# Kernel optimization log

Measured on AMD Instinct MI355X. Metric: run time of the kernel, lower is better.

## Reference

```python
import jax, jax.numpy as jnp
import numpy as np
import math

D_MODEL = 1024
N_HEADS = 16
HEAD_DIM = 64


def setup_inputs() -> dict:
    key = jax.random.key(0)
    k_x, k_q, k_k, k_v, k_o = jax.random.split(key, 5)
    lecun = jax.nn.initializers.lecun_normal()
    return {
        "x": jax.random.normal(k_x, (4, 2048, D_MODEL), dtype=jnp.float32),
        "W_q": lecun(k_q, (N_HEADS, D_MODEL, HEAD_DIM), jnp.float32),
        "W_k": lecun(k_k, (N_HEADS, D_MODEL, HEAD_DIM), jnp.float32),
        "W_v": lecun(k_v, (N_HEADS, D_MODEL, HEAD_DIM), jnp.float32),
        "W_o": lecun(k_o, (D_MODEL, D_MODEL), jnp.float32),
    }


def reference(x, W_q, W_k, W_v, W_o):
    # x: [b, l, e]; W_{q,k,v}: [h, e, d]; W_o: [e, e]
    q = jnp.einsum('ble,hed->bhld', x, W_q)
    k = jnp.einsum('ble,hed->bhld', x, W_k)
    v = jnp.einsum('ble,hed->bhld', x, W_v)
    scores = jnp.einsum('bhld,bhsd->bhls', q, k) / math.sqrt(HEAD_DIM)
    attn = jax.nn.softmax(scores, axis=-1)
    av = jnp.einsum('bhls,bhsd->bhld', attn, v)  # [b, h, l, d]
    b, h, l, d = av.shape
    concat = jnp.transpose(av, (0, 2, 1, 3)).reshape(b, l, h * d)
    out = jnp.einsum('ble,eo->blo', concat, W_o)
    return jnp.asarray(out, dtype=jnp.float32)
```

## Files before the change

### kernel.cpp

```cpp
#include <hip/hip_runtime.h>

#define BATCH 4
#define LSEQ  2048
#define DM    1024
#define NH    16
#define HD    64
#define NTOK  (BATCH * LSEQ)

typedef _Float16 f16x8 __attribute__((ext_vector_type(8)));
typedef _Float16 f16x4 __attribute__((ext_vector_type(4)));
typedef __fp16   hf16x2 __attribute__((ext_vector_type(2)));
typedef float    f32x4 __attribute__((ext_vector_type(4)));
typedef float    f32x16 __attribute__((ext_vector_type(16)));

typedef __attribute__((address_space(1))) const unsigned int GU32;
typedef __attribute__((address_space(3))) unsigned int LU32;

__device__ __forceinline__ void gload_lds16(const _Float16* g, _Float16* l)
{
    __builtin_amdgcn_global_load_lds(
        (GU32*)(unsigned long long)g,
        (LU32*)(unsigned int)(unsigned long long)l, 16, 0, 0);
}


__global__ __launch_bounds__(256) void cvt_kernel(const float* __restrict__ src,
                                                  _Float16* __restrict__ dst, int n4)
{
    int i = blockIdx.x * 256 + threadIdx.x;
    if (i >= n4) return;
    float4 v = ((const float4*)src)[i];
    f16x4 h;
    h[0] = (_Float16)v.x; h[1] = (_Float16)v.y; h[2] = (_Float16)v.z; h[3] = (_Float16)v.w;
    ((f16x4*)dst)[i] = h;
}

__global__ __launch_bounds__(256) void tconv3_kernel(
    const float* __restrict__ Wq, const float* __restrict__ Wk,
    const float* __restrict__ Wv, _Float16* __restrict__ dst)
{
    const int z = blockIdx.z;
    const int which = z >> 4, h = z & 15;
    const float* __restrict__ src =
        ((which == 0) ? Wq : (which == 1) ? Wk : Wv) + (size_t)h * DM * HD;
    _Float16* __restrict__ d = dst + (size_t)z * DM * HD;
    const int e0 = blockIdx.y * 64;
    __shared__ float Ls[64][65];
    const int t = threadIdx.x;
    #pragma unroll
    for (int j = 0; j < 4; ++j) {
        int cidx = t + j * 256;
        int row = cidx >> 4, col4 = (cidx & 15) * 4;
        float4 v = *(const float4*)&src[(size_t)(e0 + row) * HD + col4];
        Ls[row][col4] = v.x; Ls[row][col4+1] = v.y; Ls[row][col4+2] = v.z; Ls[row][col4+3] = v.w;
    }
    __syncthreads();
    const int dd = t & 63, sc = t >> 6;
    alignas(16) _Float16 tmp[16];
    #pragma unroll
    for (int i = 0; i < 16; ++i) tmp[i] = (_Float16)Ls[sc * 16 + i][dd];
    *(f16x8*)&d[(size_t)dd * DM + e0 + sc * 16]     = *(f16x8*)&tmp[0];
    *(f16x8*)&d[(size_t)dd * DM + e0 + sc * 16 + 8] = *(f16x8*)&tmp[8];
}

__global__ __launch_bounds__(256) void tconv_kernel(const float* __restrict__ src,
                                                    _Float16* __restrict__ dst, int E, int D)
{
    const int d0 = blockIdx.x * 64, e0 = blockIdx.y * 64;
    __shared__ float Ls[64][65];
    const int t = threadIdx.x;
    #pragma unroll
    for (int j = 0; j < 4; ++j) {
        int cidx = t + j * 256;
        int row = cidx >> 4, col4 = (cidx & 15) * 4;
        float4 v = *(const float4*)&src[(size_t)(e0 + row) * D + d0 + col4];
        Ls[row][col4] = v.x; Ls[row][col4+1] = v.y; Ls[row][col4+2] = v.z; Ls[row][col4+3] = v.w;
    }
    __syncthreads();
    const int dd = t & 63, sc = t >> 6;
    alignas(16) _Float16 tmp[16];
    #pragma unroll
    for (int i = 0; i < 16; ++i) tmp[i] = (_Float16)Ls[sc * 16 + i][dd];
    *(f16x8*)&dst[(size_t)(d0 + dd) * E + e0 + sc * 16]     = *(f16x8*)&tmp[0];
    *(f16x8*)&dst[(size_t)(d0 + dd) * E + e0 + sc * 16 + 8] = *(f16x8*)&tmp[8];
}

template<int MODE>
__global__ __launch_bounds__(256) void gemm_kernel(
    const _Float16* __restrict__ A, const _Float16* __restrict__ B,
    float* __restrict__ out32,
    _Float16* __restrict__ qo, _Float16* __restrict__ ko, _Float16* __restrict__ vto)
{
    const int n0 = blockIdx.x * 128, m0 = blockIdx.y * 128;
    __shared__ _Float16 As[128 * 64];
    __shared__ _Float16 Bs[128 * 64];
    const int t = threadIdx.x;
    const int lane = t & 63, w = t >> 6;
    const int quad = lane >> 4, c = lane & 15;
    const int wm = (w & 1) * 64, wn = (w >> 1) * 64;
    const int srow = lane >> 3;
    const int scol8 = ((lane & 7) ^ (lane >> 3)) * 8;

    const int colsw = (quad ^ (c & 7)) * 8;
    const _Float16* Ap0 = &As[(wm + c) * 64 + colsw];
    const _Float16* Ap1 = &As[(wm + c) * 64 + (colsw ^ 32)];
    const _Float16* Bp0 = &Bs[(wn + c) * 64 + colsw];
    const _Float16* Bp1 = &Bs[(wn + c) * 64 + (colsw ^ 32)];

    f32x4 acc[4][4];
    #pragma unroll
    for (int i = 0; i < 4; ++i)
        #pragma unroll
        for (int j = 0; j < 4; ++j) acc[i][j] = {0.f, 0.f, 0.f, 0.f};

    for (int e0 = 0; e0 < DM; e0 += 64) {
        __syncthreads();
        #pragma unroll
        for (int j = 0; j < 4; ++j) {
            int ch = w * 4 + j;
            gload_lds16(A + (size_t)(m0 + ch * 8 + srow) * DM + e0 + scol8, As + ch * 512);
            gload_lds16(B + (size_t)(n0 + ch * 8 + srow) * DM + e0 + scol8, Bs + ch * 512);
        }
        __syncthreads();
        #pragma unroll
        for (int kc = 0; kc < 2; ++kc) {
            const _Float16* Ap = kc ? Ap1 : Ap0;
            const _Float16* Bp = kc ? Bp1 : Bp0;
            f16x8 af[4], bf[4];
            #pragma unroll
            for (int mt = 0; mt < 4; ++mt) af[mt] = *(const f16x8*)(Ap + mt * 1024);
            #pragma unroll
            for (int nt = 0; nt < 4; ++nt) bf[nt] = *(const f16x8*)(Bp + nt * 1024);
            #pragma unroll
            for (int mt = 0; mt < 4; ++mt)
                #pragma unroll
                for (int nt = 0; nt < 4; ++nt)
                    acc[mt][nt] = __builtin_amdgcn_mfma_f32_16x16x32_f16(af[mt], bf[nt], acc[mt][nt], 0, 0, 0);
        }
    }

    if (MODE == 0) {
        #pragma unroll
        for (int mt = 0; mt < 4; ++mt)
            #pragma unroll
            for (int nt = 0; nt < 4; ++nt)
                #pragma unroll
                for (int r = 0; r < 4; ++r) {
                    int row = m0 + wm + mt * 16 + quad * 4 + r;
                    int col = n0 + wn + nt * 16 + c;
                    out32[(size_t)row * DM + col] = acc[mt][nt][r];
                }
    } else {
        const int mi = (n0 + wn) >> 6;
        const int which = mi >> 4, hh = mi & 15;
        if (which == 2) {
            #pragma unroll
            for (int mt = 0; mt < 4; ++mt) {
                int tokb = m0 + wm + mt * 16;
                int b = tokb >> 11;
                int l = (tokb & (LSEQ - 1)) + 8 * (quad & 1) + 4 * (quad >> 1);
                #pragma unroll
                for (int nt = 0; nt < 4; ++nt) {
                    int d = nt * 16 + c;
                    f16x4 pk;
                    pk[0] = (_Float16)acc[mt][nt][0];
                    pk[1] = (_Float16)acc[mt][nt][1];
                    pk[2] = (_Float16)acc[mt][nt][2];
                    pk[3] = (_Float16)acc[mt][nt][3];
                    *(f16x4*)&vto[((size_t)(b * NH + hh) * HD + d) * LSEQ + l] = pk;
                }
            }
        } else {
            _Float16* dst = (which == 0) ? qo : ko;
            const float vs = (which == 0) ? 0.18033688011112042f : 1.0f;
            #pragma unroll
            for (int mt = 0; mt < 4; ++mt)
                #pragma unroll
                for (int nt = 0; nt < 4; ++nt)
                    #pragma unroll
                    for (int r = 0; r < 4; ++r) {
                        int tok = m0 + wm + mt * 16 + quad * 4 + r;
                        int b = tok >> 11, l = tok & (LSEQ - 1);
                        int d = nt * 16 + c;
                        dst[((size_t)(b * NH + hh) * LSEQ + l) * HD + d] = (_Float16)(acc[mt][nt][r] * vs);
                    }
        }
    }
}

__global__ __launch_bounds__(256, 5) void attn_kernel(
    const _Float16* __restrict__ Qg, const _Float16* __restrict__ Kg,
    const _Float16* __restrict__ Vtg, _Float16* __restrict__ concat)
{
    const int bh = blockIdx.x;
    const int q0 = blockIdx.y * 128;
    const int b = bh >> 4, head = bh & (NH - 1);
    __shared__ _Float16 Ks[2][64 * 64];
    __shared__ _Float16 Vts[2][64 * 64];
    const int t = threadIdx.x;
    const int lane = t & 63, w = t >> 6;
    const int m = lane & 31, hl = lane >> 5;
    const int srow = lane >> 3;
    const int scol8 = ((lane & 7) ^ (lane >> 3)) * 8;

    f16x8 qf[4];
    #pragma unroll
    for (int kstep = 0; kstep < 4; ++kstep)
        qf[kstep] = *(const f16x8*)&Qg[((size_t)bh * LSEQ + q0 + w * 32 + m) * HD + kstep * 16 + hl * 8];

    f32x16 o[2];
    #pragma unroll
    for (int i = 0; i < 16; ++i) { o[0][i] = 0.f; o[1][i] = 0.f; }
    float lp = 0.f;
    const hf16x2 ones2 = {(__fp16)1.0f, (__fp16)1.0f};

    auto stage = [&](int bi, int s0n) {
        #pragma unroll
        for (int j = 0; j < 2; ++j) {
            int ch = w * 2 + j;
            gload_lds16(Kg  + ((size_t)bh * LSEQ + s0n + ch * 8 + srow) * HD + scol8, &Ks[bi][ch * 512]);
            gload_lds16(Vtg + ((size_t)bh * HD + ch * 8 + srow) * LSEQ + s0n + scol8, &Vts[bi][ch * 512]);
        }
    };

    constexpr int NT = LSEQ / 64;
    stage(0, 0);
    int cur = 0;

    for (int tt = 0; tt < NT; ++tt) {
        if (tt + 1 < NT) {
            stage(cur ^ 1, (tt + 1) * 64);
            asm volatile("s_waitcnt vmcnt(4)" ::: "memory");
        } else {
            asm volatile("s_waitcnt vmcnt(0)" ::: "memory");
        }
        __builtin_amdgcn_s_barrier();
        __builtin_amdgcn_sched_barrier(0);

        const _Float16* Kb = &Ks[cur][0];
        const _Float16* Vb = &Vts[cur][0];

        f16x8 pf[4];
        #pragma unroll
        for (int sblk = 0; sblk < 2; ++sblk) {
            const int rr = sblk * 32 + m;
            const int rx = rr & 7;
            const _Float16* Krow = Kb + rr * 64;
            f32x16 sT;
            #pragma unroll
            for (int i = 0; i < 16; ++i) sT[i] = 0.f;
            __builtin_amdgcn_s_setprio(1);
            #pragma unroll
            for (int kstep = 0; kstep < 4; ++kstep) {
                f16x8 kf = *(const f16x8*)(Krow + (((kstep * 2 + hl) ^ rx) * 8));
                sT = __builtin_amdgcn_mfma_f32_32x32x16_f16(kf, qf[kstep], sT, 0, 0, 0);
            }
            __builtin_amdgcn_s_setprio(0);
            union { unsigned int u[4]; f16x8 v; } P0, P1;
            #pragma unroll
            for (int q = 0; q < 8; ++q) {
                float e0 = __builtin_amdgcn_exp2f(sT[2 * q]);
                float e1 = __builtin_amdgcn_exp2f(sT[2 * q + 1]);
                union { hf16x2 h; unsigned int u; } uu;
                uu.h = __builtin_amdgcn_cvt_pkrtz(e0, e1);
                lp = __builtin_amdgcn_fdot2(uu.h, ones2, lp, false);
                if (q < 4) P0.u[q] = uu.u; else P1.u[q - 4] = uu.u;
            }
            pf[sblk * 2 + 0] = P0.v;
            pf[sblk * 2 + 1] = P1.v;
        }

        __builtin_amdgcn_s_setprio(1);
        #pragma unroll
        for (int dblk = 0; dblk < 2; ++dblk) {
            const int dd = dblk * 32 + m;
            const int dx = dd & 7;
            const _Float16* Vrow = Vb + dd * 64;
            #pragma unroll
            for (int sstep = 0; sstep < 4; ++sstep) {
                f16x8 vf = *(const f16x8*)(Vrow + (((2 * sstep + hl) ^ dx) * 8));
                o[dblk] = __builtin_amdgcn_mfma_f32_32x32x16_f16(pf[sstep], vf, o[dblk], 0, 0, 0);
            }
        }
        __builtin_amdgcn_s_setprio(0);

        asm volatile("s_waitcnt lgkmcnt(0)" ::: "memory");
        __builtin_amdgcn_s_barrier();
        cur ^= 1;
    }

    lp += __shfl_xor(lp, 32);

    #pragma unroll
    for (int rg = 0; rg < 16; ++rg) {
        const int mrow = (rg & 3) + 8 * (rg >> 2) + 4 * hl;
        const float inv = 1.f / __shfl(lp, mrow);
        const int row = q0 + w * 32 + mrow;
        #pragma unroll
        for (int dblk = 0; dblk < 2; ++dblk)
            concat[((size_t)b * LSEQ + row) * DM + head * HD + dblk * 32 + m] =
                (_Float16)(o[dblk][rg] * inv);
    }
}

extern "C" void kernel_launch(void* const* d_in, const int* in_sizes, int n_in,
                              void* d_out, int out_size, void* d_ws, size_t ws_size,
                              hipStream_t stream)
{
    (void)in_sizes; (void)n_in; (void)out_size; (void)ws_size;

    const float* x  = (const float*)d_in[0];
    const float* Wq = (const float*)d_in[1];
    const float* Wk = (const float*)d_in[2];
    const float* Wv = (const float*)d_in[3];
    const float* Wo = (const float*)d_in[4];
    float* out = (float*)d_out;

    const size_t XE = (size_t)NTOK * DM;
    const size_t WQKV = (size_t)3 * NH * HD * DM;
    _Float16* xh  = (_Float16*)d_ws;
    _Float16* WtA = xh + XE;
    _Float16* Wot = WtA + WQKV;
    _Float16* q   = Wot + (size_t)DM * DM;
    _Float16* k   = q + XE;
    _Float16* vt  = k + XE;
    _Float16* cc  = vt + XE;

    cvt_kernel<<<8192, 256, 0, stream>>>(x, xh, (int)(XE / 4));
    tconv3_kernel<<<dim3(1, 16, 48), 256, 0, stream>>>(Wq, Wk, Wv, WtA);
    tconv_kernel<<<dim3(16, 16, 1), 256, 0, stream>>>(Wo, Wot, DM, DM);

    gemm_kernel<1><<<dim3(24, 64), 256, 0, stream>>>(xh, WtA, nullptr, q, k, vt);
    attn_kernel<<<dim3(64, LSEQ / 128), 256, 0, stream>>>(q, k, vt, cc);
    gemm_kernel<0><<<dim3(8, 64), 256, 0, stream>>>(cc, Wot, out, nullptr, nullptr, nullptr);
}
```

Baseline: 288.5 us.

## Store V in MFMA-fragment layout and load it straight to registers

The QKV projection now writes V in a layout that matches the per-lane MFMA B-operand fragment order for each 64-key tile. The attention kernel then loads V directly from global memory into registers, one tile ahead, so V no longer passes through shared memory. This halves shared-memory staging, drops the second barrier per iteration, and relaxes occupancy to 4 blocks per SM. The cost is more vector registers for the prefetched V fragments and reliance on vmcnt counting to order the K and V loads correctly.

After: 275.4 us. -4.5%, faster.

```diff
diff --git a/kernel.cpp b/kernel.cpp
--- a/kernel.cpp
+++ b/kernel.cpp
@@ -157,17 +157,23 @@
             #pragma unroll
             for (int mt = 0; mt < 4; ++mt) {
                 int tokb = m0 + wm + mt * 16;
-                int b = tokb >> 11;
-                int l = (tokb & (LSEQ - 1)) + 8 * (quad & 1) + 4 * (quad >> 1);
+                int btok = tokb >> 11;
+                int lt   = tokb & (LSEQ - 1);
+                int tau  = lt >> 6, sstep = (lt >> 4) & 3;
+                int hlw  = quad & 1, jb = 4 * (quad >> 1);
+                size_t bhbase = (size_t)(btok * NH + hh) * (32 * 8 * 512);
                 #pragma unroll
                 for (int nt = 0; nt < 4; ++nt) {
                     int d = nt * 16 + c;
+                    int m2 = d & 31, dblk = d >> 5;
                     f16x4 pk;
                     pk[0] = (_Float16)acc[mt][nt][0];
                     pk[1] = (_Float16)acc[mt][nt][1];
                     pk[2] = (_Float16)acc[mt][nt][2];
                     pk[3] = (_Float16)acc[mt][nt][3];
-                    *(f16x4*)&vto[((size_t)(b * NH + hh) * HD + d) * LSEQ + l] = pk;
+                    size_t off = bhbase
+                               + ((size_t)(tau * 8 + dblk * 4 + sstep) * 64 + hlw * 32 + m2) * 8 + jb;
+                    *(f16x4*)&vto[off] = pk;
                 }
             }
         } else {
@@ -188,7 +194,7 @@
     }
 }
 
-__global__ __launch_bounds__(256, 5) void attn_kernel(
+__global__ __launch_bounds__(256, 4) void attn_kernel(
     const _Float16* __restrict__ Qg, const _Float16* __restrict__ Kg,
     const _Float16* __restrict__ Vtg, _Float16* __restrict__ concat)
 {
@@ -196,7 +202,6 @@
     const int q0 = blockIdx.y * 128;
     const int b = bh >> 4, head = bh & (NH - 1);
     __shared__ _Float16 Ks[2][64 * 64];
-    __shared__ _Float16 Vts[2][64 * 64];
     const int t = threadIdx.x;
     const int lane = t & 63, w = t >> 6;
     const int m = lane & 31, hl = lane >> 5;
@@ -218,27 +223,32 @@
         #pragma unroll
         for (int j = 0; j < 2; ++j) {
             int ch = w * 2 + j;
-            gload_lds16(Kg  + ((size_t)bh * LSEQ + s0n + ch * 8 + srow) * HD + scol8, &Ks[bi][ch * 512]);
-            gload_lds16(Vtg + ((size_t)bh * HD + ch * 8 + srow) * LSEQ + s0n + scol8, &Vts[bi][ch * 512]);
-        }
+            gload_lds16(Kg + ((size_t)bh * LSEQ + s0n + ch * 8 + srow) * HD + scol8, &Ks[bi][ch * 512]);
+        }
+    };
+
+    const _Float16* Vbase = Vtg + (size_t)bh * (32 * 8 * 512) + (size_t)lane * 8;
+    f16x8 vf[8];
+    auto loadV = [&](int tile) {
+        const _Float16* p = Vbase + (size_t)tile * 4096;
+        #pragma unroll
+        for (int q = 0; q < 8; ++q)
+            vf[q] = *(const f16x8*)(p + q * 512);
     };
 
     constexpr int NT = LSEQ / 64;
     stage(0, 0);
+    loadV(0);
     int cur = 0;
 
     for (int tt = 0; tt < NT; ++tt) {
-        if (tt + 1 < NT) {
-            stage(cur ^ 1, (tt + 1) * 64);
-            asm volatile("s_waitcnt vmcnt(4)" ::: "memory");
-        } else {
-            asm volatile("s_waitcnt vmcnt(0)" ::: "memory");
-        }
+        asm volatile("s_waitcnt vmcnt(8)" ::: "memory");
         __builtin_amdgcn_s_barrier();
         __builtin_amdgcn_sched_barrier(0);
 
+        if (tt + 1 < NT) stage(cur ^ 1, (tt + 1) * 64);
+
         const _Float16* Kb = &Ks[cur][0];
-        const _Float16* Vb = &Vts[cur][0];
 
         f16x8 pf[4];
         #pragma unroll
@@ -272,20 +282,16 @@
 
         __builtin_amdgcn_s_setprio(1);
         #pragma unroll
-        for (int dblk = 0; dblk < 2; ++dblk) {
-            const int dd = dblk * 32 + m;
-            const int dx = dd & 7;
-            const _Float16* Vrow = Vb + dd * 64;
-            #pragma unroll
-            for (int sstep = 0; sstep < 4; ++sstep) {
-                f16x8 vf = *(const f16x8*)(Vrow + (((2 * sstep + hl) ^ dx) * 8));
-                o[dblk] = __builtin_amdgcn_mfma_f32_32x32x16_f16(pf[sstep], vf, o[dblk], 0, 0, 0);
-            }
-        }
+        for (int dblk = 0; dblk < 2; ++dblk)
+            #pragma unroll
+            for (int sstep = 0; sstep < 4; ++sstep)
+                o[dblk] = __builtin_amdgcn_mfma_f32_32x32x16_f16(pf[sstep], vf[dblk * 4 + sstep], o[dblk], 0, 0, 0);
         __builtin_amdgcn_s_setprio(0);
 
+        if (tt + 1 < NT) loadV(tt + 1);
+
         asm volatile("s_waitcnt lgkmcnt(0)" ::: "memory");
-        __builtin_amdgcn_s_barrier();
+        __builtin_amdgcn_sched_barrier(0);
         cur ^= 1;
     }
 
```
